# Kernel optimization log

Hardware: AMD Instinct MI355X
Metric: run time of the kernel (lower is better)

The kernel has to match this reference:

```python
import jax, jax.numpy as jnp
import numpy as np

HID = 128      # hidden_features
NF = 32        # noise_features
NPL = NF // 4  # noise features per layer
RES = 512      # noise grid resolution
N = 262144     # number of query points


def leaky_relu(x):
    return jax.nn.leaky_relu(x, negative_slope=0.01)


def sample_bilinear(image, coords):
    """image: [M, H, W]; coords: [..., M, 2] -> [..., M]"""
    M, Hn, Wn = image.shape
    x = coords[..., 0] - 0.5
    y = coords[..., 1] - 0.5
    x0f = jnp.floor(x)
    y0f = jnp.floor(y)
    xw = x - x0f
    yw = y - y0f
    x0 = x0f.astype(jnp.int32) % Wn
    x1 = (x0f.astype(jnp.int32) + 1) % Wn
    y0 = y0f.astype(jnp.int32) % Hn
    y1 = (y0f.astype(jnp.int32) + 1) % Hn
    f = jnp.arange(M)  # broadcasts against [..., M] index arrays
    i00 = image[f, y0, x0]
    i01 = image[f, y0, x1]
    i10 = image[f, y1, x0]
    i11 = image[f, y1, x1]
    i0 = i00 + (i01 - i00) * xw
    i1 = i10 + (i11 - i10) * xw
    return i0 + (i1 - i0) * yw


def setup_inputs() -> dict:
    key = jax.random.key(0)
    ks = jax.random.split(key, 12)
    noise = jax.random.normal(ks[0], (NF, RES, RES), dtype=jnp.float32)
    coords = jax.random.normal(ks[1], (N, 2), dtype=jnp.float32)
    # NoiseTransforms param: randn * 0.05 * 2**i per feature
    scale = 0.05 * (2.0 ** np.arange(NF)).astype(np.float32)
    transformations = jax.random.normal(ks[2], (NF, 2, 2), dtype=jnp.float32) * scale[:, None, None]
    input_vec = jnp.ones((HID,), dtype=jnp.float32)
    s_lin = 1.0 / np.sqrt(HID)
    s_noise = 1.0 / np.sqrt(NPL)
    lw = jax.random.uniform(ks[3], (4, HID, HID), jnp.float32, -s_lin, s_lin)
    lb = jax.random.uniform(ks[4], (4, HID), jnp.float32, -s_lin, s_lin)
    lnw = jax.random.uniform(ks[5], (4, HID, NPL), jnp.float32, -s_noise, s_noise)
    tw1 = jax.random.uniform(ks[6], (HID, HID), jnp.float32, -s_lin, s_lin)
    tb1 = jax.random.uniform(ks[7], (HID,), jnp.float32, -s_lin, s_lin)
    tw2 = jax.random.uniform(ks[8], (1, HID), jnp.float32, -s_lin, s_lin)
    tb2 = jax.random.uniform(ks[9], (1,), jnp.float32, -s_lin, s_lin)
    return {"noise": noise, "coords": coords, "transformations": transformations,
            "input_vec": input_vec, "lw": lw, "lb": lb, "lnw": lnw,
            "tw1": tw1, "tb1": tb1, "tw2": tw2, "tb2": tb2}


def reference(noise, coords, transformations, input_vec, lw, lb, lnw, tw1, tb1, tw2, tb2):
    # noise coords: [..., NF, 2]
    noise_coords = jnp.einsum('...n,Mmn->...Mm', coords, transformations)
    noise_values = sample_bilinear(noise, noise_coords)  # [..., NF]
    x = input_vec  # [HID], broadcasts up through layer adds
    for i in range(4):
        nv = noise_values[..., i * NPL:(i + 1) * NPL]
        x = leaky_relu(jnp.einsum('...h,oh->...o', x, lw[i]) + lb[i]
                       + jnp.einsum('...n,on->...o', nv, lnw[i]))
    h = leaky_relu(jnp.einsum('...h,oh->...o', x, tw1) + tb1)
    return jnp.einsum('...h,oh->...o', h, tw2) + tb2  # [..., 1]
```

## Files before the change

### kernel.cpp

```cpp
#include <hip/hip_runtime.h>

typedef _Float16 f16;
typedef f16 f16x4 __attribute__((ext_vector_type(4)));
typedef f16 f16x8 __attribute__((ext_vector_type(8)));
typedef float f32x4 __attribute__((ext_vector_type(4)));

#define RES 512
#define PTS 128
#define XS  136
#define AS  16


__device__ __forceinline__
void pack_w_body(int g, const float* __restrict__ lw, const float* __restrict__ lnw,
                 const float* __restrict__ lb, const float* __restrict__ tw1,
                 const float* __restrict__ tb1, const float* __restrict__ ivec,
                 f16* __restrict__ wf, f16* __restrict__ waugf) {
    if (g < 10240) {
        const int L = g >> 11, r = g & 2047;
        const int lane = r & 63, frag = r >> 6;
        const int q = lane >> 4, l15 = lane & 15;
        const int mt = frag >> 2, c = frag & 3;
        const float* src = ((L < 4) ? (lw + L * 16384) : tw1)
                           + (mt * 16 + l15) * 128 + c * 32 + q * 8;
        f16x8 h;
        #pragma unroll
        for (int j = 0; j < 8; ++j) h[j] = (f16)src[j];
        *(f16x8*)(wf + (size_t)g * 8) = h;
    } else {
        const int ga = g - 10240;
        const int L = ga >> 9, r = ga & 511;
        const int lane = r & 63, mt = r >> 6;
        const int q = lane >> 4, l15 = lane & 15;
        const int row = mt * 16 + l15;
        f16x4 h = {};
        if (L < 4 && q < 2) {
            const float* src = lnw + L * 1024 + row * 8 + q * 4;
            #pragma unroll
            for (int j = 0; j < 4; ++j) h[j] = (f16)src[j];
        }
        if (q == 2) {
            if (L == 0) {
                float s = lb[row];
                const float4* w4 = (const float4*)(lw + row * 128);
                const float4* v4 = (const float4*)ivec;
                #pragma unroll 8
                for (int k = 0; k < 32; ++k) {
                    const float4 w = w4[k], v = v4[k];
                    s += w.x * v.x + w.y * v.y + w.z * v.z + w.w * v.w;
                }
                h[0] = (f16)s;
            } else {
                h[0] = (f16)((L < 4) ? lb[L * 128 + row] : tb1[row]);
            }
        }
        *(f16x4*)(waugf + (size_t)ga * 4) = h;
    }
}

__global__ __launch_bounds__(256)
void pack_all_k(const float* __restrict__ n, f16* __restrict__ q,
                const float* __restrict__ lw,  const float* __restrict__ lnw,
                const float* __restrict__ lb,  const float* __restrict__ tw1,
                const float* __restrict__ tb1, const float* __restrict__ ivec,
                f16* __restrict__ wf, f16* __restrict__ waugf) {
    const int b = blockIdx.x;
    if (b < 8192) {
        const int idx = b * 256 + threadIdx.x;
        const int qx = idx & 255, rest = idx >> 8;
        const int qy = rest & 255, m = rest >> 8;
        const float* src = n + ((size_t)m * 512 + 2 * qy) * 512 + 2 * qx;
        const float2 r0 = *(const float2*)(src);
        const float2 r1 = *(const float2*)(src + 512);
        f16x4 o; o[0]=(f16)r0.x; o[1]=(f16)r0.y; o[2]=(f16)r1.x; o[3]=(f16)r1.y;
        *(f16x4*)(q + (size_t)idx * 4) = o;
    } else {
        pack_w_body((b - 8192) * 256 + threadIdx.x, lw, lnw, lb, tw1, tb1, ivec, wf, waugf);
    }
}

__global__ __launch_bounds__(256)
void pack_w_k(const float* __restrict__ lw,  const float* __restrict__ lnw,
              const float* __restrict__ lb,  const float* __restrict__ tw1,
              const float* __restrict__ tb1, const float* __restrict__ ivec,
              f16* __restrict__ wf, f16* __restrict__ waugf) {
    pack_w_body(blockIdx.x * 256 + threadIdx.x, lw, lnw, lb, tw1, tb1, ivec, wf, waugf);
}

__device__ __forceinline__ float quad_tap(uint2 q, int sy, int sx) {
    unsigned w = sy ? q.y : q.x;
    w >>= (sx << 4);
    union { unsigned short u; f16 h; } cv; cv.u = (unsigned short)w;
    return (float)cv.h;
}

template <bool QUAD>
__global__ __launch_bounds__(256, 4)
void sample_kernel(const void* __restrict__ noise_v,
                   const float* __restrict__ coords,
                   const float* __restrict__ trans,
                   f16* __restrict__ nv_ws, const int Ntot)
{
    __shared__ float T_sh[128];
    const int t = threadIdx.x;
    if (t < 128) T_sh[t] = trans[t];
    __syncthreads();

    const int g = blockIdx.x & 7;
    const int pb = (blockIdx.x >> 3) * 1024 + t;

    int mk[4];
    if (g < 7) { mk[0] = g; mk[1] = g + 9; mk[2] = g + 17; mk[3] = g + 25; }
    else       { mk[0] = 7; mk[1] = 8;     mk[2] = 16;     mk[3] = 24;     }

    float2 c[4];
    #pragma unroll
    for (int j = 0; j < 4; ++j)
        c[j] = *(const float2*)(coords + (pb + 256 * j) * 2);

    float nvr[4][4];
    {
        #pragma clang fp contract(off)
        #pragma unroll
        for (int j = 0; j < 4; ++j) {
            const float cx = c[j].x;
            const float cy = c[j].y;
            #pragma unroll
            for (int k = 0; k < 4; ++k) {
                const int m = mk[k];
                const float T00 = T_sh[m*4+0], T01 = T_sh[m*4+1];
                const float T10 = T_sh[m*4+2], T11 = T_sh[m*4+3];
                const float p0x = T00 * cx;
                const float p0y = T10 * cx;
                const float ncx = __builtin_fmaf(T01, cy, p0x);
                const float ncy = __builtin_fmaf(T11, cy, p0y);
                const float u = ncx - 0.5f;
                const float v = ncy - 0.5f;
                const float xf = floorf(u), yf = floorf(v);
                const float xw = u - xf, yw = v - yf;
                int ix = (xf >= 2147483648.0f || xf < -2147483648.0f) ? (int)(-2147483647 - 1) : (int)xf;
                int iy = (yf >= 2147483648.0f || yf < -2147483648.0f) ? (int)(-2147483647 - 1) : (int)yf;
                const int x0 = ix & (RES - 1);
                const int x1 = (int)(((unsigned)ix + 1u) & (unsigned)(RES - 1));
                const int y0 = iy & (RES - 1);
                const int y1 = (int)(((unsigned)iy + 1u) & (unsigned)(RES - 1));
                float i00, i01, i10, i11;
                if constexpr (QUAD) {
                    const f16* pl = (const f16*)noise_v + (size_t)m * (256 * 256 * 4);
                    const int qx0 = x0 >> 1, sx0 = x0 & 1;
                    const int qx1 = x1 >> 1, sx1 = x1 & 1;
                    const int qy0 = y0 >> 1, sy0 = y0 & 1;
                    const int qy1 = y1 >> 1, sy1 = y1 & 1;
                    const uint2 qa = *(const uint2*)(pl + (qy0 * 256 + qx0) * 4);
                    const uint2 qb = *(const uint2*)(pl + (qy0 * 256 + qx1) * 4);
                    const uint2 qc = *(const uint2*)(pl + (qy1 * 256 + qx0) * 4);
                    const uint2 qd = *(const uint2*)(pl + (qy1 * 256 + qx1) * 4);
                    i00 = quad_tap(qa, sy0, sx0);
                    i01 = quad_tap(qb, sy0, sx1);
                    i10 = quad_tap(qc, sy1, sx0);
                    i11 = quad_tap(qd, sy1, sx1);
                } else {
                    const float* pl = (const float*)noise_v + (size_t)m * (RES * RES);
                    i00 = pl[y0 * RES + x0];
                    i01 = pl[y0 * RES + x1];
                    i10 = pl[y1 * RES + x0];
                    i11 = pl[y1 * RES + x1];
                }
                const float a0 = i00 + (i01 - i00) * xw;
                const float a1 = i10 + (i11 - i10) * xw;
                nvr[j][k] = a0 + (a1 - a0) * yw;
            }
        }
    }
    #pragma unroll
    for (int j = 0; j < 4; ++j) {
        #pragma unroll
        for (int k = 0; k < 4; ++k) {
            const int m = mk[k];
            const int slot = (m & 7) * 4 + (m >> 3);
            nv_ws[(size_t)slot * Ntot + pb + 256 * j] = (f16)nvr[j][k];
        }
    }
}

__global__ __launch_bounds__(256, 2)
void mlp_kernel(const f16* __restrict__ nv_ws,
                const f16* __restrict__ wf,
                const f16* __restrict__ waugf,
                const float* __restrict__ tw2,
                const float* __restrict__ tb2,
                float* __restrict__ out, const int Ntot)
{
    __shared__ f16 Wm[16384];
    __shared__ f16 Waug[2048];
    __shared__ f16 xa[PTS * XS];
    __shared__ f16 xaug[PTS * AS];
    __shared__ __align__(16) float tw2_sh[128];
    __shared__ float pp[2][PTS];

    const int t    = threadIdx.x;
    const int wave = t >> 6;
    const int lane = t & 63;
    const int q    = lane >> 4;
    const int l15  = lane & 15;
    const int wi   = wave >> 1;
    const int wj   = wave & 1;
    const int pbase = blockIdx.x * PTS;
    const int p = t >> 1, h = t & 1;

    if (t < 128) {
        tw2_sh[t] = tw2[t];
        xaug[t * AS + 8] = (f16)1.0f;
        #pragma unroll
        for (int c = 9; c < 16; ++c) xaug[t * AS + c] = (f16)0.0f;
    }
    const float tb2_0 = tb2[0];

    f16x8 nva, nvb;
    {
        const int P = pbase + p;
        #pragma unroll
        for (int j = 0; j < 8; ++j) {
            nva[j] = nv_ws[(size_t)(j * 4 + 2 * h)     * Ntot + P];
            nvb[j] = nv_ws[(size_t)(j * 4 + 2 * h + 1) * Ntot + P];
        }
    }
    if (h == 0) *(f16x8*)&xaug[p * AS] = nva;

    *(f16x8*)&Waug[t * 8] = *(const f16x8*)&waugf[t * 8];
    __syncthreads();

    const f32x4 z4 = {0.f, 0.f, 0.f, 0.f};
    f32x4 acc[4][4];
    f16x8 wreg[8], areg;
    #pragma unroll 1
    for (int L = 0; L < 5; ++L) {
        if (L < 4) {
            const f16* wsrc = wf + (L + 1) * 16384;
            #pragma unroll
            for (int i = 0; i < 8; ++i)
                wreg[i] = *(const f16x8*)&wsrc[(t + i * 256) * 8];
            areg = *(const f16x8*)&waugf[(size_t)(L + 1) * 2048 + t * 8];
        }

        if (L == 0) {
            #pragma unroll
            for (int pg = 0; pg < 4; ++pg)
                #pragma unroll
                for (int mtl = 0; mtl < 4; ++mtl) acc[pg][mtl] = z4;
        }
        __builtin_amdgcn_s_setprio(1);
        if (L) {
            #pragma unroll
            for (int c = 0; c < 4; ++c) {
                const int kc = c * 32 + q * 8;
                f16x8 xb[4];
                #pragma unroll
                for (int pg = 0; pg < 4; ++pg)
                    xb[pg] = *(const f16x8*)&xa[(wi * 64 + pg * 16 + l15) * XS + kc];
                #pragma unroll
                for (int mtl = 0; mtl < 4; ++mtl) {
                    const f16x8 aw = *(const f16x8*)
                        &Wm[(((wj * 4 + mtl) * 4 + c) * 64 + lane) * 8];
                    #pragma unroll
                    for (int pg = 0; pg < 4; ++pg) {
                        const f32x4 ci = (c == 0) ? z4 : acc[pg][mtl];
                        acc[pg][mtl] = __builtin_amdgcn_mfma_f32_16x16x32_f16(aw, xb[pg], ci, 0, 0, 0);
                    }
                }
            }
        }
        {
            f16x4 xb4[4];
            #pragma unroll
            for (int pg = 0; pg < 4; ++pg)
                xb4[pg] = *(const f16x4*)&xaug[(wi * 64 + pg * 16 + l15) * AS + q * 4];
            #pragma unroll
            for (int mtl = 0; mtl < 4; ++mtl) {
                const f16x4 awa = *(const f16x4*)&Waug[((wj * 4 + mtl) * 64 + lane) * 4];
                #pragma unroll
                for (int pg = 0; pg < 4; ++pg)
                    acc[pg][mtl] = __builtin_amdgcn_mfma_f32_16x16x16f16(
                        awa, xb4[pg], acc[pg][mtl], 0, 0, 0);
            }
        }
        __builtin_amdgcn_s_setprio(0);

        if (L < 4) {
            f16x4 hv[4][4];
            #pragma unroll
            for (int pg = 0; pg < 4; ++pg)
                #pragma unroll
                for (int mtl = 0; mtl < 4; ++mtl)
                    #pragma unroll
                    for (int r = 0; r < 4; ++r) {
                        float v = acc[pg][mtl][r];
                        v = fmaxf(v, 0.01f * v);
                        hv[pg][mtl][r] = (f16)v;
                    }
            __syncthreads();
            #pragma unroll
            for (int pg = 0; pg < 4; ++pg) {
                const int pr = (wi * 64 + pg * 16 + l15) * XS;
                #pragma unroll
                for (int mtl = 0; mtl < 4; ++mtl)
                    *(f16x4*)&xa[pr + wj * 64 + mtl * 16 + q * 4] = hv[pg][mtl];
            }
            if (L < 3) {
                const int Ln = L + 1;
                if ((Ln >> 1) == h)
                    *(f16x8*)&xaug[p * AS] = (Ln & 1) ? nvb : nva;
            }
            {
                #pragma unroll
                for (int i = 0; i < 8; ++i)
                    *(f16x8*)&Wm[(t + i * 256) * 8] = wreg[i];
                *(f16x8*)&Waug[t * 8] = areg;
            }
            __syncthreads();
        } else {
            #pragma unroll
            for (int pg = 0; pg < 4; ++pg) {
                float s = 0.f;
                #pragma unroll
                for (int mtl = 0; mtl < 4; ++mtl) {
                    const f32x4 w4 = *(const f32x4*)&tw2_sh[wj * 64 + mtl * 16 + q * 4];
                    #pragma unroll
                    for (int r = 0; r < 4; ++r) {
                        float v = acc[pg][mtl][r];
                        v = fmaxf(v, 0.01f * v);
                        s += w4[r] * v;
                    }
                }
                s += __shfl_xor(s, 16);
                s += __shfl_xor(s, 32);
                if (q == 0) pp[wj][wi * 64 + pg * 16 + l15] = s;
            }
            __syncthreads();
            if (t < 128)
                out[pbase + t] = pp[0][t] + pp[1][t] + tb2_0;
        }
    }
}

extern "C" void kernel_launch(void* const* d_in, const int* in_sizes, int n_in,
                              void* d_out, int out_size, void* d_ws, size_t ws_size,
                              hipStream_t stream) {
    const float* noise  = (const float*)d_in[0];
    const float* coords = (const float*)d_in[1];
    const float* trans  = (const float*)d_in[2];
    const float* ivec   = (const float*)d_in[3];
    const float* lw     = (const float*)d_in[4];
    const float* lb     = (const float*)d_in[5];
    const float* lnw    = (const float*)d_in[6];
    const float* tw1    = (const float*)d_in[7];
    const float* tb1    = (const float*)d_in[8];
    const float* tw2    = (const float*)d_in[9];
    const float* tb2    = (const float*)d_in[10];
    float* o            = (float*)d_out;

    const int N = in_sizes[1] / 2;
    f16* nv    = (f16*)d_ws;
    const size_t NV = (size_t)N * 32;
    f16* wfp   = nv + NV;
    f16* waugp = wfp + 5 * 16384;
    f16* qn    = waugp + 5 * 2048;
    const size_t need_full = (NV + 5 * 16384 + 5 * 2048
                              + (size_t)32 * 256 * 256 * 4) * sizeof(f16);

    if (ws_size >= need_full) {
        pack_all_k<<<8192 + 50, 256, 0, stream>>>(noise, qn, lw, lnw, lb, tw1, tb1,
                                                  ivec, wfp, waugp);
        sample_kernel<true><<<(N / 1024) * 8, 256, 0, stream>>>(qn, coords, trans, nv, N);
    } else {
        pack_w_k<<<50, 256, 0, stream>>>(lw, lnw, lb, tw1, tb1, ivec, wfp, waugp);
        sample_kernel<false><<<(N / 1024) * 8, 256, 0, stream>>>(noise, coords, trans, nv, N);
    }
    mlp_kernel<<<N / PTS, 256, 0, stream>>>(nv, wfp, waugp, tw2, tb2, o, N);
}
```

Measured before the change: 206.5 us.

## Tile quad-packed noise into 4x8 blocks, double points per sampler block, pad AS

The noise pre-pack now has each thread read a 4x8 patch with float4 loads and write eight 2x2 quads contiguously. Quads are stored in 2x4 tiles so that taps near each other in 2D share cache lines. The sampler gives each thread 8 points instead of 4, halving the grid and exposing more independent gathers per thread at the cost of registers. AS padding in the MLP changes from 16 to 20, presumably to reduce LDS bank conflicts.

```diff
diff --git a/kernel.cpp b/kernel.cpp
--- a/kernel.cpp
+++ b/kernel.cpp
@@ -8,7 +8,7 @@
 #define RES 512
 #define PTS 128
 #define XS  136
-#define AS  16
+#define AS  20
 
 
 __device__ __forceinline__
@@ -65,17 +65,31 @@
                 const float* __restrict__ tb1, const float* __restrict__ ivec,
                 f16* __restrict__ wf, f16* __restrict__ waugf) {
     const int b = blockIdx.x;
-    if (b < 8192) {
+    if (b < 1024) {
         const int idx = b * 256 + threadIdx.x;
-        const int qx = idx & 255, rest = idx >> 8;
-        const int qy = rest & 255, m = rest >> 8;
-        const float* src = n + ((size_t)m * 512 + 2 * qy) * 512 + 2 * qx;
-        const float2 r0 = *(const float2*)(src);
-        const float2 r1 = *(const float2*)(src + 512);
-        f16x4 o; o[0]=(f16)r0.x; o[1]=(f16)r0.y; o[2]=(f16)r1.x; o[3]=(f16)r1.y;
-        *(f16x4*)(q + (size_t)idx * 4) = o;
+        const int tx = idx & 63, rest = idx >> 6;
+        const int ty = rest & 127, m = rest >> 7;
+        const float* src = n + ((size_t)m * 512 + 4 * ty) * 512 + 8 * tx;
+        f16 row[4][8];
+        #pragma unroll
+        for (int r = 0; r < 4; ++r) {
+            const float4 a = *(const float4*)(src + r * 512);
+            const float4 c = *(const float4*)(src + r * 512 + 4);
+            row[r][0]=(f16)a.x; row[r][1]=(f16)a.y; row[r][2]=(f16)a.z; row[r][3]=(f16)a.w;
+            row[r][4]=(f16)c.x; row[r][5]=(f16)c.y; row[r][6]=(f16)c.z; row[r][7]=(f16)c.w;
+        }
+        f16* dst = q + (size_t)idx * 32;
+        #pragma unroll
+        for (int qr = 0; qr < 2; ++qr)
+            #pragma unroll
+            for (int qc = 0; qc < 4; ++qc) {
+                f16x4 o;
+                o[0] = row[2*qr][2*qc];   o[1] = row[2*qr][2*qc+1];
+                o[2] = row[2*qr+1][2*qc]; o[3] = row[2*qr+1][2*qc+1];
+                *(f16x4*)(dst + (qr * 4 + qc) * 4) = o;
+            }
     } else {
-        pack_w_body((b - 8192) * 256 + threadIdx.x, lw, lnw, lb, tw1, tb1, ivec, wf, waugf);
+        pack_w_body((b - 1024) * 256 + threadIdx.x, lw, lnw, lb, tw1, tb1, ivec, wf, waugf);
     }
 }
 
@@ -107,22 +121,22 @@
     __syncthreads();
 
     const int g = blockIdx.x & 7;
-    const int pb = (blockIdx.x >> 3) * 1024 + t;
+    const int pb = (blockIdx.x >> 3) * 2048 + t;
 
     int mk[4];
     if (g < 7) { mk[0] = g; mk[1] = g + 9; mk[2] = g + 17; mk[3] = g + 25; }
     else       { mk[0] = 7; mk[1] = 8;     mk[2] = 16;     mk[3] = 24;     }
 
-    float2 c[4];
+    float2 c[8];
     #pragma unroll
-    for (int j = 0; j < 4; ++j)
+    for (int j = 0; j < 8; ++j)
         c[j] = *(const float2*)(coords + (pb + 256 * j) * 2);
 
-    float nvr[4][4];
+    float nvr[8][4];
     {
         #pragma clang fp contract(off)
         #pragma unroll
-        for (int j = 0; j < 4; ++j) {
+        for (int j = 0; j < 8; ++j) {
             const float cx = c[j].x;
             const float cy = c[j].y;
             #pragma unroll
@@ -151,10 +165,14 @@
                     const int qx1 = x1 >> 1, sx1 = x1 & 1;
                     const int qy0 = y0 >> 1, sy0 = y0 & 1;
                     const int qy1 = y1 >> 1, sy1 = y1 & 1;
-                    const uint2 qa = *(const uint2*)(pl + (qy0 * 256 + qx0) * 4);
-                    const uint2 qb = *(const uint2*)(pl + (qy0 * 256 + qx1) * 4);
-                    const uint2 qc = *(const uint2*)(pl + (qy1 * 256 + qx0) * 4);
-                    const uint2 qd = *(const uint2*)(pl + (qy1 * 256 + qx1) * 4);
+                    const int ry0 = (qy0 >> 1) * 512 + (qy0 & 1) * 4;
+                    const int ry1 = (qy1 >> 1) * 512 + (qy1 & 1) * 4;
+                    const int cx0 = (qx0 >> 2) * 8 + (qx0 & 3);
+                    const int cx1 = (qx1 >> 2) * 8 + (qx1 & 3);
+                    const uint2 qa = *(const uint2*)(pl + (ry0 + cx0) * 4);
+                    const uint2 qb = *(const uint2*)(pl + (ry0 + cx1) * 4);
+                    const uint2 qc = *(const uint2*)(pl + (ry1 + cx0) * 4);
+                    const uint2 qd = *(const uint2*)(pl + (ry1 + cx1) * 4);
                     i00 = quad_tap(qa, sy0, sx0);
                     i01 = quad_tap(qb, sy0, sx1);
                     i10 = quad_tap(qc, sy1, sx0);
@@ -173,7 +191,7 @@
         }
     }
     #pragma unroll
-    for (int j = 0; j < 4; ++j) {
+    for (int j = 0; j < 8; ++j) {
         #pragma unroll
         for (int k = 0; k < 4; ++k) {
             const int m = mk[k];
@@ -369,12 +387,12 @@
                               + (size_t)32 * 256 * 256 * 4) * sizeof(f16);
 
     if (ws_size >= need_full) {
-        pack_all_k<<<8192 + 50, 256, 0, stream>>>(noise, qn, lw, lnw, lb, tw1, tb1,
+        pack_all_k<<<1024 + 50, 256, 0, stream>>>(noise, qn, lw, lnw, lb, tw1, tb1,
                                                   ivec, wfp, waugp);
-        sample_kernel<true><<<(N / 1024) * 8, 256, 0, stream>>>(qn, coords, trans, nv, N);
+        sample_kernel<true><<<(N / 2048) * 8, 256, 0, stream>>>(qn, coords, trans, nv, N);
     } else {
         pack_w_k<<<50, 256, 0, stream>>>(lw, lnw, lb, tw1, tb1, ivec, wfp, waugp);
-        sample_kernel<false><<<(N / 1024) * 8, 256, 0, stream>>>(noise, coords, trans, nv, N);
+        sample_kernel<false><<<(N / 2048) * 8, 256, 0, stream>>>(noise, coords, trans, nv, N);
     }
     mlp_kernel<<<N / PTS, 256, 0, stream>>>(nv, wfp, waugp, tw2, tb2, o, N);
 }
```

New measurement: 208.7 us. Within noise of the previous version (+1.1%).
